# Kernel optimization log

Measured on AMD Instinct MI355X. Metric: run time of the kernel, lower is better.

Reference implementation:

```python
import jax, jax.numpy as jnp
import numpy as np

N_NODES = 100000
D = 256
B = 2048
U = 8192
R = 8
EPS = 1e-10
AVG_NEIGHBORS = 10.0  # matches num_sample_train=10


def setup_inputs() -> dict:
    key = jax.random.key(0)
    k1, k2, k3, k4, k5, k6 = jax.random.split(key, 6)
    nodes = jax.random.randint(k1, (B,), 0, N_NODES)
    unique_idx = jax.random.randint(k2, (U,), 0, N_NODES)
    # sparse binary relational masks: ~10 sampled neighbors per node per relation
    masks = jax.random.bernoulli(k3, AVG_NEIGHBORS / U, (R, B, U)).astype(jnp.float32)
    embeddings = jax.random.normal(k4, (N_NODES, D), dtype=jnp.float32)
    weight = jax.random.normal(k5, (D, D), dtype=jnp.float32) * (1.0 / np.sqrt(D))
    rel_weights = jax.random.normal(k6, (R, D, D), dtype=jnp.float32) * (1.0 / np.sqrt(D))
    return {"nodes": nodes, "unique_idx": unique_idx, "masks": masks,
            "embeddings": embeddings, "weight": weight, "rel_weights": rel_weights}


def reference(nodes, unique_idx, masks, embeddings, weight, rel_weights):
    # self path: E[nodes] @ W.T  -> [B, D]
    self_out = embeddings[nodes] @ weight.T
    # row-normalize masks by neighbor count (+eps), as in forward_bmm
    norm_masks = masks / (masks.sum(axis=2, keepdims=True) + EPS)  # [R, B, U]
    neigh_emb = embeddings[unique_idx]  # [U, D]
    # per-relation mean aggregation: masks.bmm(neigh_emb) -> [R, B, D]
    agg = jnp.einsum('rbu,ud->rbd', norm_masks, neigh_emb)
    # combine across relations with relation-specific weights and sum: [B, D]
    rel_out = jnp.einsum('rbd,rod->bo', agg, rel_weights)
    return jax.nn.relu(self_out + rel_out)
```

## Files before the change

kernel.cpp:

```cpp
#include <hip/hip_runtime.h>
#include <hip/hip_bf16.h>

constexpr int D      = 256;
constexpr int Bn     = 2048;
constexpr int U      = 8192;
constexpr int R      = 8;
constexpr int KEXT   = R * D + D;
constexpr float EPS  = 1e-10f;
constexpr int CAP    = 256;

typedef __attribute__((ext_vector_type(8))) short bf16x8;
typedef __attribute__((ext_vector_type(4))) float f32x4;
typedef __attribute__((ext_vector_type(4))) unsigned int u32x4;

__global__ __launch_bounds__(256) void build_wt(const float* __restrict__ weight,
                                                const float* __restrict__ relw,
                                                __hip_bfloat16* __restrict__ w2) {
    const int o = blockIdx.x;
    const int t = threadIdx.x;
    #pragma unroll
    for (int c = 0; c < 9; ++c) {
        float v;
        if (c < 8) v = relw[((size_t)(c * D + o)) * D + t];
        else       v = weight[(size_t)o * D + t];
        w2[(size_t)o * KEXT + c * D + t] = __float2bfloat16(v);
    }
}

__global__ __launch_bounds__(256) void scan_agg(const int*   __restrict__ nodes,
                                                const int*   __restrict__ uidx,
                                                const float* __restrict__ masks,
                                                const float* __restrict__ emb,
                                                __hip_bfloat16* __restrict__ A) {
    __shared__ int s_cnt;
    __shared__ int s_u[CAP];
    __shared__ int s_nid[CAP];

    const int tid = threadIdx.x;
    const int bid = blockIdx.x;

    if (bid < R * Bn) {
        if (tid == 0) s_cnt = 0;
        __syncthreads();

        const u32x4* row = (const u32x4*)(masks + (size_t)bid * U);
        unsigned flags = 0u;
        #pragma unroll
        for (int j = 0; j < U / 1024; ++j) {
            u32x4 m = __builtin_nontemporal_load(&row[j * 256 + tid]);
            unsigned f = (m.x ? 1u : 0u) | (m.y ? 2u : 0u) |
                         (m.z ? 4u : 0u) | (m.w ? 8u : 0u);
            flags |= f << (4 * j);
        }

        if (flags) {
            unsigned fl = flags;
            do {
                int bit = __builtin_ctz(fl);
                fl &= fl - 1;
                int j = bit >> 2, c = bit & 3;
                int u = (j * 256 + tid) * 4 + c;
                int p = atomicAdd(&s_cnt, 1);
                if (p < CAP) s_u[p] = u;
            } while (fl);
        }
        __syncthreads();

        const int total = s_cnt;
        const int cnt = total < CAP ? total : CAP;
        if (tid < cnt) s_nid[tid] = uidx[s_u[tid]];
        __syncthreads();

        const float scale = 1.0f / ((float)total + EPS);

        float a0 = 0.f, a1 = 0.f, a2 = 0.f, a3 = 0.f;
        int k = 0;
        for (; k + 4 <= cnt; k += 4) {
            a0 += emb[(size_t)s_nid[k]     * D + tid];
            a1 += emb[(size_t)s_nid[k + 1] * D + tid];
            a2 += emb[(size_t)s_nid[k + 2] * D + tid];
            a3 += emb[(size_t)s_nid[k + 3] * D + tid];
        }
        for (; k < cnt; ++k) a0 += emb[(size_t)s_nid[k] * D + tid];

        const int r = bid >> 11;
        const int b = bid & (Bn - 1);
        A[(size_t)b * KEXT + r * D + tid] =
            __float2bfloat16(((a0 + a1) + (a2 + a3)) * scale);
    } else {
        const int b = bid - R * Bn;
        const int node = nodes[b];
        A[(size_t)b * KEXT + R * D + tid] = __float2bfloat16(emb[(size_t)node * D + tid]);
    }
}

constexpr int SK = 72;

__global__ __launch_bounds__(256) void gemm_mfma(const __hip_bfloat16* __restrict__ A,
                                                 const __hip_bfloat16* __restrict__ W2,
                                                 float* __restrict__ out) {
    __shared__ ushort As[64 * SK];
    __shared__ ushort Bs[64 * SK];

    const int tid  = threadIdx.x;
    const int lane = tid & 63;
    const int wave = tid >> 6;
    const int wm   = wave >> 1;
    const int wn   = wave & 1;
    const int quad = lane >> 4;
    const int rrow = lane & 15;

    const int bn = blockIdx.x * 64;
    const int bm = blockIdx.y * 64;

    const int kq = tid & 7;
    const int m0 = tid >> 3;

    f32x4 acc[2][2];
    #pragma unroll
    for (int i = 0; i < 2; ++i)
        #pragma unroll
        for (int j = 0; j < 2; ++j) acc[i][j] = (f32x4){0.f, 0.f, 0.f, 0.f};

    const ushort* Ag = (const ushort*)A;
    const ushort* Bg = (const ushort*)W2;

    for (int bk = 0; bk < KEXT; bk += 64) {
        *(uint4*)&As[m0 * SK + kq * 8] =
            *(const uint4*)&Ag[(size_t)(bm + m0) * KEXT + bk + kq * 8];
        *(uint4*)&As[(m0 + 32) * SK + kq * 8] =
            *(const uint4*)&Ag[(size_t)(bm + m0 + 32) * KEXT + bk + kq * 8];
        *(uint4*)&Bs[m0 * SK + kq * 8] =
            *(const uint4*)&Bg[(size_t)(bn + m0) * KEXT + bk + kq * 8];
        *(uint4*)&Bs[(m0 + 32) * SK + kq * 8] =
            *(const uint4*)&Bg[(size_t)(bn + m0 + 32) * KEXT + bk + kq * 8];

        __syncthreads();

        #pragma unroll
        for (int kc = 0; kc < 2; ++kc) {
            bf16x8 a0 = *(const bf16x8*)&As[(wm * 32 +  0 + rrow) * SK + kc * 32 + quad * 8];
            bf16x8 a1 = *(const bf16x8*)&As[(wm * 32 + 16 + rrow) * SK + kc * 32 + quad * 8];
            bf16x8 b0 = *(const bf16x8*)&Bs[(wn * 32 +  0 + rrow) * SK + kc * 32 + quad * 8];
            bf16x8 b1 = *(const bf16x8*)&Bs[(wn * 32 + 16 + rrow) * SK + kc * 32 + quad * 8];
            acc[0][0] = __builtin_amdgcn_mfma_f32_16x16x32_bf16(a0, b0, acc[0][0], 0, 0, 0);
            acc[0][1] = __builtin_amdgcn_mfma_f32_16x16x32_bf16(a0, b1, acc[0][1], 0, 0, 0);
            acc[1][0] = __builtin_amdgcn_mfma_f32_16x16x32_bf16(a1, b0, acc[1][0], 0, 0, 0);
            acc[1][1] = __builtin_amdgcn_mfma_f32_16x16x32_bf16(a1, b1, acc[1][1], 0, 0, 0);
        }

        __syncthreads();
    }

    #pragma unroll
    for (int tm = 0; tm < 2; ++tm) {
        #pragma unroll
        for (int tn = 0; tn < 2; ++tn) {
            const int col = bn + wn * 32 + tn * 16 + rrow;
            #pragma unroll
            for (int reg = 0; reg < 4; ++reg) {
                const int row = bm + wm * 32 + tm * 16 + quad * 4 + reg;
                out[(size_t)row * 256 + col] = fmaxf(acc[tm][tn][reg], 0.f);
            }
        }
    }
}

extern "C" void kernel_launch(void* const* d_in, const int* in_sizes, int n_in,
                              void* d_out, int out_size, void* d_ws, size_t ws_size,
                              hipStream_t stream) {
    const int*   nodes  = (const int*)  d_in[0];
    const int*   uidx   = (const int*)  d_in[1];
    const float* masks  = (const float*)d_in[2];
    const float* emb    = (const float*)d_in[3];
    const float* weight = (const float*)d_in[4];
    const float* relw   = (const float*)d_in[5];
    float* out = (float*)d_out;

    __hip_bfloat16* A  = (__hip_bfloat16*)d_ws;
    __hip_bfloat16* W2 = A + (size_t)Bn * KEXT;

    build_wt<<<D, 256, 0, stream>>>(weight, relw, W2);
    scan_agg<<<R * Bn + Bn, 256, 0, stream>>>(nodes, uidx, masks, emb, A);
    gemm_mfma<<<dim3(4, 32), 256, 0, stream>>>(A, W2, out);
}
```

Baseline: 756.7 us.

## Split mask scan and embedding gather into separate kernels with wave-per-row gather

The fused scan+aggregate kernel is split in two. A scan kernel streams the masks and writes neighbor ids into a global per-row list using global atomics. A gather kernel then uses one wave per row with float4 loads and shuffled ids to sum the embeddings. This is meant to keep the memory-bound mask scan from stalling on the dependent gather latency and to raise gather efficiency. In exchange it adds a kernel launch, global atomics, and a neighbor-list cap of 64, so any row with more than 64 neighbors would silently drop the extras.

```diff
diff --git a/kernel.cpp b/kernel.cpp
--- a/kernel.cpp
+++ b/kernel.cpp
@@ -7,15 +7,21 @@
 constexpr int R      = 8;
 constexpr int KEXT   = R * D + D;
 constexpr float EPS  = 1e-10f;
-constexpr int CAP    = 256;
+constexpr int LCAP   = 64;
 
 typedef __attribute__((ext_vector_type(8))) short bf16x8;
 typedef __attribute__((ext_vector_type(4))) float f32x4;
 typedef __attribute__((ext_vector_type(4))) unsigned int u32x4;
 
+__device__ __forceinline__ ushort bf16bits(float x) {
+    __hip_bfloat16 h = __float2bfloat16(x);
+    return __builtin_bit_cast(ushort, h);
+}
+
 __global__ __launch_bounds__(256) void build_wt(const float* __restrict__ weight,
                                                 const float* __restrict__ relw,
-                                                __hip_bfloat16* __restrict__ w2) {
+                                                __hip_bfloat16* __restrict__ w2,
+                                                int* __restrict__ cnt) {
     const int o = blockIdx.x;
     const int t = threadIdx.x;
     #pragma unroll
@@ -25,72 +31,92 @@
         else       v = weight[(size_t)o * D + t];
         w2[(size_t)o * KEXT + c * D + t] = __float2bfloat16(v);
     }
-}
-
-__global__ __launch_bounds__(256) void scan_agg(const int*   __restrict__ nodes,
-                                                const int*   __restrict__ uidx,
-                                                const float* __restrict__ masks,
-                                                const float* __restrict__ emb,
-                                                __hip_bfloat16* __restrict__ A) {
-    __shared__ int s_cnt;
-    __shared__ int s_u[CAP];
-    __shared__ int s_nid[CAP];
-
+    const int g = o * 256 + t;
+    if (g < R * Bn) cnt[g] = 0;
+}
+
+__global__ __launch_bounds__(256) void scan(const float* __restrict__ masks,
+                                            const int*   __restrict__ uidx,
+                                            int* __restrict__ cnt,
+                                            int* __restrict__ list) {
     const int tid = threadIdx.x;
     const int bid = blockIdx.x;
 
-    if (bid < R * Bn) {
-        if (tid == 0) s_cnt = 0;
-        __syncthreads();
-
-        const u32x4* row = (const u32x4*)(masks + (size_t)bid * U);
-        unsigned flags = 0u;
-        #pragma unroll
-        for (int j = 0; j < U / 1024; ++j) {
-            u32x4 m = __builtin_nontemporal_load(&row[j * 256 + tid]);
-            unsigned f = (m.x ? 1u : 0u) | (m.y ? 2u : 0u) |
-                         (m.z ? 4u : 0u) | (m.w ? 8u : 0u);
-            flags |= f << (4 * j);
+    const u32x4* row = (const u32x4*)(masks + (size_t)bid * U);
+    unsigned flags = 0u;
+    #pragma unroll
+    for (int j = 0; j < U / 1024; ++j) {
+        u32x4 m = __builtin_nontemporal_load(&row[j * 256 + tid]);
+        unsigned f = (m.x ? 1u : 0u) | (m.y ? 2u : 0u) |
+                     (m.z ? 4u : 0u) | (m.w ? 8u : 0u);
+        flags |= f << (4 * j);
+    }
+
+    if (flags) {
+        unsigned fl = flags;
+        do {
+            int bit = __builtin_ctz(fl);
+            fl &= fl - 1;
+            int u = ((bit >> 2) * 256 + tid) * 4 + (bit & 3);
+            int nid = uidx[u];
+            int p = atomicAdd(&cnt[bid], 1);
+            if (p < LCAP) list[(size_t)bid * LCAP + p] = nid;
+        } while (fl);
+    }
+}
+
+__global__ __launch_bounds__(256) void gather(const int*   __restrict__ nodes,
+                                              const float* __restrict__ emb,
+                                              const int*   __restrict__ cnt,
+                                              const int*   __restrict__ list,
+                                              __hip_bfloat16* __restrict__ A) {
+    const int lane = threadIdx.x & 63;
+    const int row  = blockIdx.x * 4 + (threadIdx.x >> 6);
+    ushort* Au = (ushort*)A;
+
+    if (row < R * Bn) {
+        const int   n     = cnt[row];
+        const int   m     = n < LCAP ? n : LCAP;
+        const float scale = 1.0f / ((float)n + EPS);
+
+        int mynid = 0;
+        if (lane < m) mynid = list[(size_t)row * LCAP + lane];
+
+        f32x4 a0 = {0.f,0.f,0.f,0.f}, a1 = a0, a2 = a0, a3 = a0;
+        for (int k = 0; k < m; k += 4) {
+            const int i1 = (k + 1 < m) ? k + 1 : m - 1;
+            const int i2 = (k + 2 < m) ? k + 2 : m - 1;
+            const int i3 = (k + 3 < m) ? k + 3 : m - 1;
+            const int n0 = __shfl(mynid, k);
+            const int n1 = __shfl(mynid, i1);
+            const int n2 = __shfl(mynid, i2);
+            const int n3 = __shfl(mynid, i3);
+            f32x4 e0 = *(const f32x4*)&emb[(size_t)n0 * D + lane * 4];
+            f32x4 e1 = *(const f32x4*)&emb[(size_t)n1 * D + lane * 4];
+            f32x4 e2 = *(const f32x4*)&emb[(size_t)n2 * D + lane * 4];
+            f32x4 e3 = *(const f32x4*)&emb[(size_t)n3 * D + lane * 4];
+            a0 += e0;
+            if (k + 1 < m) a1 += e1;
+            if (k + 2 < m) a2 += e2;
+            if (k + 3 < m) a3 += e3;
         }
-
-        if (flags) {
-            unsigned fl = flags;
-            do {
-                int bit = __builtin_ctz(fl);
-                fl &= fl - 1;
-                int j = bit >> 2, c = bit & 3;
-                int u = (j * 256 + tid) * 4 + c;
-                int p = atomicAdd(&s_cnt, 1);
-                if (p < CAP) s_u[p] = u;
-            } while (fl);
-        }
-        __syncthreads();
-
-        const int total = s_cnt;
-        const int cnt = total < CAP ? total : CAP;
-        if (tid < cnt) s_nid[tid] = uidx[s_u[tid]];
-        __syncthreads();
-
-        const float scale = 1.0f / ((float)total + EPS);
-
-        float a0 = 0.f, a1 = 0.f, a2 = 0.f, a3 = 0.f;
-        int k = 0;
-        for (; k + 4 <= cnt; k += 4) {
-            a0 += emb[(size_t)s_nid[k]     * D + tid];
-            a1 += emb[(size_t)s_nid[k + 1] * D + tid];
-            a2 += emb[(size_t)s_nid[k + 2] * D + tid];
-            a3 += emb[(size_t)s_nid[k + 3] * D + tid];
-        }
-        for (; k < cnt; ++k) a0 += emb[(size_t)s_nid[k] * D + tid];
-
-        const int r = bid >> 11;
-        const int b = bid & (Bn - 1);
-        A[(size_t)b * KEXT + r * D + tid] =
-            __float2bfloat16(((a0 + a1) + (a2 + a3)) * scale);
+        f32x4 s = (a0 + a1) + (a2 + a3);
+        s.x *= scale; s.y *= scale; s.z *= scale; s.w *= scale;
+
+        const int r = row >> 11;
+        const int b = row & (Bn - 1);
+        ushort4 o;
+        o.x = bf16bits(s.x); o.y = bf16bits(s.y);
+        o.z = bf16bits(s.z); o.w = bf16bits(s.w);
+        *(ushort4*)&Au[(size_t)b * KEXT + r * D + lane * 4] = o;
     } else {
-        const int b = bid - R * Bn;
+        const int b    = row - R * Bn;
         const int node = nodes[b];
-        A[(size_t)b * KEXT + R * D + tid] = __float2bfloat16(emb[(size_t)node * D + tid]);
+        f32x4 e = *(const f32x4*)&emb[(size_t)node * D + lane * 4];
+        ushort4 o;
+        o.x = bf16bits(e.x); o.y = bf16bits(e.y);
+        o.z = bf16bits(e.z); o.w = bf16bits(e.w);
+        *(ushort4*)&Au[(size_t)b * KEXT + R * D + lane * 4] = o;
     }
 }
 
@@ -179,8 +205,11 @@
 
     __hip_bfloat16* A  = (__hip_bfloat16*)d_ws;
     __hip_bfloat16* W2 = A + (size_t)Bn * KEXT;
-
-    build_wt<<<D, 256, 0, stream>>>(weight, relw, W2);
-    scan_agg<<<R * Bn + Bn, 256, 0, stream>>>(nodes, uidx, masks, emb, A);
+    int* cnt  = (int*)(W2 + (size_t)D * KEXT);
+    int* list = cnt + R * Bn;
+
+    build_wt<<<D, 256, 0, stream>>>(weight, relw, W2, cnt);
+    scan<<<R * Bn, 256, 0, stream>>>(masks, uidx, cnt, list);
+    gather<<<(R * Bn + Bn) / 4, 256, 0, stream>>>(nodes, emb, cnt, list, A);
     gemm_mfma<<<dim3(4, 32), 256, 0, stream>>>(A, W2, out);
 }
```

Measured after the change: 761.9 us. No clear change (+0.7%).
